# Kernel optimization log

Hardware: AMD Instinct MI355X
Metric: run time of the kernel (lower is better)

## Reference

```python
import jax, jax.numpy as jnp
import numpy as np
import math

IN_FEATURES = 512
RFF_FEATURES = 2048
OUT_FEATURES = 1000
N = 8192
RIDGE_PENALTY = 1.0
MEAN_FIELD_FACTOR = 25.0
RFF_SCALAR = math.sqrt(RFF_FEATURES / 2)  # 32.0


def _random_ortho(key, n, m):
    q, _ = jnp.linalg.qr(jax.random.normal(key, (n, m), dtype=jnp.float32))
    return q


def setup_inputs() -> dict:
    key = jax.random.key(0)
    k_d, k_w, k_norm, k_b, k_lw, k_lb, k_cov = jax.random.split(key, 7)
    D = jax.random.normal(k_d, (N, IN_FEATURES), dtype=jnp.float32)
    # RFF weight: concat of random orthonormal blocks (rff_features > in_features)
    ws = []
    dim_left = RFF_FEATURES
    kk = k_w
    while dim_left > IN_FEATURES:
        kk, sub = jax.random.split(kk)
        ws.append(_random_ortho(sub, IN_FEATURES, IN_FEATURES))
        dim_left -= IN_FEATURES
    kk, sub = jax.random.split(kk)
    ws.append(_random_ortho(sub, IN_FEATURES, dim_left))
    W = jnp.concatenate(ws, axis=1)  # [in, rff]
    feature_norm = jax.random.normal(k_norm, W.shape, dtype=jnp.float32) ** 2
    W = W * jnp.sqrt(feature_norm.sum(0))
    b = jax.random.uniform(k_b, (RFF_FEATURES,), dtype=jnp.float32) * (2.0 * math.pi)
    # logit head (nn.Linear): weight [out, rff], bias [out]
    bound = 1.0 / math.sqrt(RFF_FEATURES)
    logit_w = jax.random.uniform(k_lw, (OUT_FEATURES, RFF_FEATURES), dtype=jnp.float32,
                                 minval=-bound, maxval=bound)
    logit_b = jax.random.uniform(k_lb, (OUT_FEATURES,), dtype=jnp.float32,
                                 minval=-bound, maxval=bound)
    # positive-definite covariance buffer (stand-in for inverted precision)
    A = jax.random.normal(k_cov, (RFF_FEATURES, RFF_FEATURES), dtype=jnp.float32) * 0.01
    covariance = A @ A.T + jnp.eye(RFF_FEATURES, dtype=jnp.float32)
    return {"D": D, "W": W, "b": b, "logit_w": logit_w, "logit_b": logit_b,
            "covariance": covariance}


def reference(D, W, b, logit_w, logit_b, covariance):
    # RFF feature map: cos(D @ W + b) / rff_scalar  -> [N, rff]
    Phi = jnp.cos(D @ W + b) / RFF_SCALAR
    # linear head -> [N, out]
    pred = Phi @ logit_w.T + logit_b
    # diag(Phi @ cov @ Phi.T) * ridge computed row-wise in O(N*r^2)
    diag_cov = jnp.sum((Phi @ covariance) * Phi, axis=-1) * RIDGE_PENALTY  # [N]
    logits_scale = jnp.sqrt(1.0 + diag_cov * MEAN_FIELD_FACTOR)
    return pred / logits_scale[:, None]
```

## Files before the change

kernel.cpp:

```cpp
#include <hip/hip_runtime.h>
#include <hip/hip_fp8.h>
#include <math.h>

#define N_ROWS 8192
#define IN_F   512
#define RFF    2048
#define OUT_F  1000
#define OUT_PAD 1024
#define INV_RFF_SCALAR 0.03125f
#define MEAN_FIELD 25.0f
#define PHI_NT 24

typedef __attribute__((ext_vector_type(8))) short short8;
typedef __attribute__((ext_vector_type(4))) float f32x4;
typedef __attribute__((ext_vector_type(2))) long long2v;

__device__ __forceinline__ unsigned short f32_to_bf16(float f) {
    unsigned u = __float_as_uint(f);
    unsigned r = 0x7FFFu + ((u >> 16) & 1u);
    return (unsigned short)((u + r) >> 16);
}
__device__ __forceinline__ float bf16_to_f32(unsigned short h) {
    return __uint_as_float(((unsigned)h) << 16);
}
__device__ __forceinline__ unsigned char f32_to_fp8(float x) {
    __hip_fp8_e4m3 q(x);
    return (unsigned char)q.__x;
}

__device__ __forceinline__ int perm64(int k) {
    return (k & ~63) | (((k >> 3) & 3) << 4) | (((k >> 5) & 1) << 3) | (k & 7);
}

__device__ __forceinline__ void stage_tile8(const unsigned char* __restrict__ X,
                                            int r0, int k0b, unsigned char* lds,
                                            int w, int lane) {
    #pragma unroll
    for (int h = 0; h < 4; ++h) {
        int qb = h * 256 + w * 64;
        int q = qb + lane;
        int rt = q >> 7, c = (q >> 4) & 7, r = q & 15;
        const void* g = X + (size_t)(r0 + rt * 16 + r) * RFF + k0b + c * 16;
        __builtin_amdgcn_global_load_lds(
            (const __attribute__((address_space(1))) void*)g,
            (__attribute__((address_space(3))) void*)(lds + qb * 16),
            16, 0, 0);
    }
}

__device__ __forceinline__ void stage_tile64(const unsigned short* __restrict__ X,
                                             int r0, int k0, unsigned char* lds,
                                             int w, int lane) {
    #pragma unroll
    for (int h = 0; h < 4; ++h) {
        int qb = h * 256 + w * 64;
        int q = qb + lane;
        int rt = q >> 7, c = (q >> 4) & 7, r = q & 15;
        const void* g = X + (size_t)(r0 + rt * 16 + r) * RFF + k0 + c * 8;
        __builtin_amdgcn_global_load_lds(
            (const __attribute__((address_space(1))) void*)g,
            (__attribute__((address_space(3))) void*)(lds + qb * 16),
            16, 0, 0);
    }
}

__global__ __launch_bounds__(256) void mega_conv_kernel(
    const float* __restrict__ D, const float* __restrict__ W,
    const float* __restrict__ Lw, const float* __restrict__ cov,
    unsigned short* __restrict__ Dh, unsigned short* __restrict__ Dl,
    unsigned short* __restrict__ Wth, unsigned short* __restrict__ Wtl,
    unsigned short* __restrict__ Lw16, unsigned char* __restrict__ CovU8,
    float* __restrict__ Cd)
{
    __shared__ float tile[64][65];
    const int bid = blockIdx.x;
    const int tid = threadIdx.x;

    if (bid < 4096) {
        int i = bid * 256 + tid;
        float4 v = ((const float4*)D)[i];
        ushort4 h, l;
        h.x = f32_to_bf16(v.x); l.x = f32_to_bf16(v.x - bf16_to_f32(h.x));
        h.y = f32_to_bf16(v.y); l.y = f32_to_bf16(v.y - bf16_to_f32(h.y));
        h.z = f32_to_bf16(v.z); l.z = f32_to_bf16(v.z - bf16_to_f32(h.z));
        h.w = f32_to_bf16(v.w); l.w = f32_to_bf16(v.w - bf16_to_f32(h.w));
        ((ushort4*)Dh)[i] = h;
        ((ushort4*)Dl)[i] = l;
    } else if (bid < 4352) {
        int b = bid - 4096;
        const int n0 = (b & 31) * 64;
        const int k0 = (b >> 5) * 64;
        #pragma unroll
        for (int i = 0; i < 16; ++i) {
            int e = i * 256 + tid;
            int r = e >> 6, c = e & 63;
            tile[r][c] = W[(size_t)(k0 + r) * RFF + n0 + c];
        }
        __syncthreads();
        #pragma unroll
        for (int i = 0; i < 16; ++i) {
            int e = i * 256 + tid;
            int r = e >> 6, c = e & 63;
            float v = tile[c][r];
            unsigned short h = f32_to_bf16(v);
            unsigned short l = f32_to_bf16(v - bf16_to_f32(h));
            Wth[(size_t)(n0 + r) * IN_F + k0 + c] = h;
            Wtl[(size_t)(n0 + r) * IN_F + k0 + c] = l;
        }
    } else if (bid < 6400) {
        int i = (bid - 4352) * 256 + tid;
        int base = i * 4;
        int row = base >> 11;
        ushort4 o;
        if (row < OUT_F) {
            float4 v = ((const float4*)Lw)[i];
            o.x = f32_to_bf16(v.x); o.y = f32_to_bf16(v.y);
            o.z = f32_to_bf16(v.z); o.w = f32_to_bf16(v.w);
        } else {
            o.x = o.y = o.z = o.w = 0;
        }
        ((ushort4*)Lw16)[i] = o;
    } else {
        int i = (bid - 6400) * 256 + tid;
        int base = i * 4;
        int row = base >> 11;
        int col = base & 2047;
        int bn = row >> 7, bk = col >> 7;
        float w = (bk < bn) ? 16.0f : (bk == bn ? 8.0f : 0.0f);
        float4 v = ((const float4*)cov)[i];
        float vv[4] = {v.x, v.y, v.z, v.w};
        float wj[4];
        #pragma unroll
        for (int j = 0; j < 4; ++j) {
            if (col + j == row) { wj[j] = 0.0f; Cd[row] = vv[j]; }
            else wj[j] = w;
        }
        uchar4 o;
        o.x = f32_to_fp8(vv[0] * wj[0]); o.y = f32_to_fp8(vv[1] * wj[1]);
        o.z = f32_to_fp8(vv[2] * wj[2]); o.w = f32_to_fp8(vv[3] * wj[3]);
        *(uchar4*)(CovU8 + (size_t)row * RFF + perm64(col)) = o;
    }
}

__global__ __launch_bounds__(256) void conv_phi8_kernel(
    const unsigned short* __restrict__ Phi16, unsigned char* __restrict__ Phi8)
{
    int i = blockIdx.x * 256 + threadIdx.x;
    int base = i * 4;
    int row = base >> 11;
    int col = base & 2047;
    ushort4 v = ((const ushort4*)Phi16)[i];
    uchar4 o;
    o.x = f32_to_fp8(bf16_to_f32(v.x) * 32.0f);
    o.y = f32_to_fp8(bf16_to_f32(v.y) * 32.0f);
    o.z = f32_to_fp8(bf16_to_f32(v.z) * 32.0f);
    o.w = f32_to_fp8(bf16_to_f32(v.w) * 32.0f);
    *(uchar4*)(Phi8 + (size_t)row * RFF + perm64(col)) = o;
}


__device__ __forceinline__ void gload16u(const void* g, unsigned short* lds) {
    __builtin_amdgcn_global_load_lds(
        (const __attribute__((address_space(1))) void*)g,
        (__attribute__((address_space(3))) void*)lds, 16, 0, 0);
}

__device__ __forceinline__ void stage_ab(const unsigned short* __restrict__ src,
                                         int stride, int r0v, int kk,
                                         unsigned short* ldsbuf,
                                         int Qa, int h, int w, int lane) {
    int q   = w * 64 + lane;
    int RT  = h * 8 + Qa * 4 + (q >> 7);
    int c   = (q >> 4) & 7, r = q & 15;
    const void* g = src + (size_t)(r0v + RT * 16 + r) * stride + kk + c * 8;
    int RTu = h * 8 + Qa * 4 + (w >> 1);
    int cu  = (w & 1) * 4;
    gload16u(g, ldsbuf + RTu * 1024 + cu * 128);
}

__device__ __forceinline__ void stageB_g(const unsigned short* __restrict__ src,
                                         int cc0, int kk, unsigned short* ldsbuf,
                                         int nh, int h, int w, int lane) {
    int q    = w * 64 + lane;
    int i    = q >> 7;
    int RTp  = (i >> 1) * 4 + nh * 2 + (i & 1);
    int c    = (q >> 4) & 7, r = q & 15;
    const void* g = src + (size_t)(cc0 + h * 128 + RTp * 16 + r) * IN_F + kk + c * 8;
    int iu   = w >> 1;
    int RTpu = (iu >> 1) * 4 + nh * 2 + (iu & 1);
    int RTu  = h * 8 + RTpu;
    int cu   = (w & 1) * 4;
    gload16u(g, ldsbuf + RTu * 1024 + cu * 128);
}

#define SB0() __builtin_amdgcn_sched_barrier(0)
#define BARRIER() do { SB0(); __builtin_amdgcn_s_barrier(); SB0(); } while (0)
#define WAITVM(N) do { asm volatile("s_waitcnt vmcnt(" #N ")"); SB0(); } while (0)


#define READ_FA(FA, mh) do {                                                  \
    _Pragma("unroll")                                                         \
    for (int i_ = 0; i_ < 4; ++i_) {                                          \
        FA[i_][0] = *(const short8*)(A + (wm * 8 + (mh) * 4 + i_) * 1024      \
                                       + quad * 128 + ln * 8);                \
        FA[i_][1] = *(const short8*)(A + (wm * 8 + (mh) * 4 + i_) * 1024      \
                                       + 512 + quad * 128 + ln * 8);          \
    } } while (0)

#define READ_FB(FB, nh) do {                                                  \
    _Pragma("unroll")                                                         \
    for (int j_ = 0; j_ < 2; ++j_) {                                          \
        FB[j_][0] = *(const short8*)(B + (wn * 4 + (nh) * 2 + j_) * 1024      \
                                       + quad * 128 + ln * 8);                \
        FB[j_][1] = *(const short8*)(B + (wn * 4 + (nh) * 2 + j_) * 1024      \
                                       + 512 + quad * 128 + ln * 8);          \
    } } while (0)

#define MFMA16(MH, NH, FA, FB) do {                                           \
    __builtin_amdgcn_s_setprio(1);                                            \
    _Pragma("unroll")                                                         \
    for (int s_ = 0; s_ < 2; ++s_)                                            \
        _Pragma("unroll")                                                     \
        for (int i_ = 0; i_ < 4; ++i_)                                        \
            _Pragma("unroll")                                                 \
            for (int j_ = 0; j_ < 2; ++j_)                                    \
                acc[(MH) * 4 + i_][(NH) * 2 + j_] =                           \
                    __builtin_amdgcn_mfma_f32_16x16x32_bf16(                  \
                        FA[i_][s_], FB[j_][s_],                               \
                        acc[(MH) * 4 + i_][(NH) * 2 + j_], 0, 0, 0);          \
    __builtin_amdgcn_s_setprio(0);                                            \
} while (0)

__global__ __launch_bounds__(512, 2) void phi_mfma8p_kernel(
    const unsigned short* __restrict__ Dh, const unsigned short* __restrict__ Dl,
    const unsigned short* __restrict__ Wth, const unsigned short* __restrict__ Wtl,
    const float* __restrict__ bias, unsigned short* __restrict__ Phi)
{
    __shared__ unsigned short ldsA[2 * 16384];
    __shared__ unsigned short ldsB[2 * 16384];
    const int tid = threadIdx.x;
    const int w = tid >> 6, lane = tid & 63;
    const int wm = w >> 2, wn = w & 3;
    const int quad = lane >> 4, ln = lane & 15;

    const int bid = blockIdx.x;
    const int xcd = bid & 7, idx = bid >> 3;
    const int rb = (xcd >> 1) * 8 + (idx & 7);
    const int cb = (xcd & 1) * 4 + (idx >> 3);
    const int r0 = rb * 256;
    const int c0 = cb * 256;

    f32x4 acc[8][4];
    #pragma unroll
    for (int i = 0; i < 8; ++i)
        #pragma unroll
        for (int j = 0; j < 4; ++j)
            acc[i][j] = (f32x4)(0.0f);

    stage_ab(Dh, IN_F, r0, 0, ldsA, 0, 0, w, lane);
    stage_ab(Dh, IN_F, r0, 0, ldsA, 0, 1, w, lane);
    stage_ab(Dh, IN_F, r0, 0, ldsA, 1, 0, w, lane);
    stage_ab(Dh, IN_F, r0, 0, ldsA, 1, 1, w, lane);
    stageB_g(Wth, c0, 0, ldsB, 0, 0, w, lane);
    stageB_g(Wth, c0, 0, ldsB, 0, 1, w, lane);
    stageB_g(Wth, c0, 0, ldsB, 1, 0, w, lane);
    stageB_g(Wth, c0, 0, ldsB, 1, 1, w, lane);
    stage_ab(Dh, IN_F, r0, 64, ldsA + 16384, 0, 0, w, lane);
    stage_ab(Dh, IN_F, r0, 64, ldsA + 16384, 0, 1, w, lane);
    stageB_g(Wth, c0, 64, ldsB + 16384, 0, 0, w, lane);
    stageB_g(Wth, c0, 64, ldsB + 16384, 0, 1, w, lane);
    WAITVM(4);
    BARRIER();

    for (int t = 0; t < PHI_NT - 1; ++t) {
        const int buf = t & 1;
        const unsigned short* A = ldsA + buf * 16384;
        const unsigned short* B = ldsB + buf * 16384;
        unsigned short* curA = ldsA + buf * 16384;
        unsigned short* curB = ldsB + buf * 16384;
        unsigned short* othA = ldsA + (buf ^ 1) * 16384;
        unsigned short* othB = ldsB + (buf ^ 1) * 16384;
        const bool has2 = (t + 2) < PHI_NT;
        const int k1 = (t + 1) * 64, k2 = (t + 2) * 64;
        const int kk1 = k1 & 511, kk2 = k2 & 511;
        const unsigned short* A1 = (k1 >= 1024) ? Dl : Dh;
        const unsigned short* B1 = (k1 >= 1024) ? Wth : (k1 >= 512 ? Wtl : Wth);
        const unsigned short* A2 = (k2 >= 1024) ? Dl : Dh;
        const unsigned short* B2 = (k2 >= 1024) ? Wth : (k2 >= 512 ? Wtl : Wth);

        short8 fa[4][2], fb0[2][2], fb1[2][2];

        READ_FA(fa, 0);
        READ_FB(fb0, 0);
        stage_ab(A1, IN_F, r0, kk1, othA, 1, 0, w, lane);
        stage_ab(A1, IN_F, r0, kk1, othA, 1, 1, w, lane);
        BARRIER();
        MFMA16(0, 0, fa, fb0);
        BARRIER();

        READ_FB(fb1, 1);
        stageB_g(B1, c0, kk1, othB, 1, 0, w, lane);
        stageB_g(B1, c0, kk1, othB, 1, 1, w, lane);
        BARRIER();
        MFMA16(0, 1, fa, fb1);
        BARRIER();

        READ_FA(fa, 1);
        if (has2) { stage_ab(A2, IN_F, r0, kk2, curA, 0, 0, w, lane);
                    stage_ab(A2, IN_F, r0, kk2, curA, 0, 1, w, lane); }
        BARRIER();
        MFMA16(1, 0, fa, fb0);
        BARRIER();

        if (has2) { stageB_g(B2, c0, kk2, curB, 0, 0, w, lane);
                    stageB_g(B2, c0, kk2, curB, 0, 1, w, lane);
                    WAITVM(4); }
        else      { WAITVM(0); }
        BARRIER();
        MFMA16(1, 1, fa, fb1);
        BARRIER();
    }

    {
        asm volatile("" ::: "memory");
        const unsigned short* A = ldsA + ((PHI_NT - 1) & 1) * 16384;
        const unsigned short* B = ldsB + ((PHI_NT - 1) & 1) * 16384;
        short8 fa[4][2], fb0[2][2], fb1[2][2];
        READ_FA(fa, 0);
        READ_FB(fb0, 0);
        READ_FB(fb1, 1);
        MFMA16(0, 0, fa, fb0);
        MFMA16(0, 1, fa, fb1);
        READ_FA(fa, 1);
        MFMA16(1, 0, fa, fb0);
        MFMA16(1, 1, fa, fb1);
    }

    float bv[4];
    #pragma unroll
    for (int nt = 0; nt < 4; ++nt)
        bv[nt] = bias[c0 + wn * 64 + nt * 16 + ln];
    #pragma unroll
    for (int mt = 0; mt < 8; ++mt)
        #pragma unroll
        for (int nt = 0; nt < 4; ++nt) {
            int col = c0 + wn * 64 + nt * 16 + ln;
            #pragma unroll
            for (int reg = 0; reg < 4; ++reg) {
                int row = r0 + wm * 128 + mt * 16 + quad * 4 + reg;
                float z = acc[mt][nt][reg] + bv[nt];
                float p = __cosf(z) * INV_RFF_SCALAR;
                Phi[(size_t)row * RFF + col] = f32_to_bf16(p);
            }
        }
}

__global__ __launch_bounds__(256) void fused_dp_kernel(
    const unsigned char* __restrict__ Phi8, const unsigned char* __restrict__ CovU8,
    const unsigned short* __restrict__ Phi16, const float* __restrict__ Cd,
    float* __restrict__ diag, const unsigned short* __restrict__ Lw,
    float* __restrict__ out)
{
    __shared__ __align__(16) unsigned char ldsA[16384];
    __shared__ __align__(16) unsigned char ldsB[16384];
    const int bid = blockIdx.x;
    const int tid = threadIdx.x;
    const int w = tid >> 6, lane = tid & 63;
    const int wm = w >> 1, wn = w & 1;
    const int quad = lane >> 4, ln = lane & 15;
    const int m3 = bid % 3;

    if (m3 == 2) {
        const int pidx = bid / 3;
        const int r0 = (pidx >> 3) * 128;
        const int c0 = (pidx & 7) * 128;

        f32x4 acc[4][4];
        #pragma unroll
        for (int i = 0; i < 4; ++i)
            #pragma unroll
            for (int j = 0; j < 4; ++j)
                acc[i][j] = (f32x4)(0.0f);

        for (int k0 = 0; k0 < RFF; k0 += 64) {
            __syncthreads();
            stage_tile64(Phi16, r0, k0, ldsA, w, lane);
            stage_tile64(Lw,    c0, k0, ldsB, w, lane);
            __syncthreads();

            #pragma unroll
            for (int s = 0; s < 2; ++s) {
                short8 fa[4], fb[4];
                #pragma unroll
                for (int t = 0; t < 4; ++t) {
                    fa[t] = *(const short8*)(ldsA + (((wm * 4 + t) * 128 + (s * 4 + quad) * 16 + ln) << 4));
                    fb[t] = *(const short8*)(ldsB + (((wn * 4 + t) * 128 + (s * 4 + quad) * 16 + ln) << 4));
                }
                #pragma unroll
                for (int mt = 0; mt < 4; ++mt)
                    #pragma unroll
                    for (int nt = 0; nt < 4; ++nt)
                        acc[mt][nt] = __builtin_amdgcn_mfma_f32_16x16x32_bf16(
                            fa[mt], fb[nt], acc[mt][nt], 0, 0, 0);
            }
        }

        #pragma unroll
        for (int mt = 0; mt < 4; ++mt)
            #pragma unroll
            for (int nt = 0; nt < 4; ++nt) {
                int col = c0 + wn * 64 + nt * 16 + ln;
                if (col < OUT_F) {
                    #pragma unroll
                    for (int reg = 0; reg < 4; ++reg) {
                        int row = r0 + wm * 64 + mt * 16 + quad * 4 + reg;
                        out[(size_t)row * OUT_F + col] = acc[mt][nt][reg];
                    }
                }
            }
    } else {
        const int didx = (bid / 3) * 2 + m3;
        const int J = 15 - (didx & 15);
        const int r0 = (didx >> 4) * 128;
        const int c0 = J * 128;
        const int kmax = (J + 1) * 128;

        f32x4 acc[4][4];
        #pragma unroll
        for (int i = 0; i < 4; ++i)
            #pragma unroll
            for (int j = 0; j < 4; ++j)
                acc[i][j] = (f32x4)(0.0f);

        for (int k0 = 0; k0 < kmax; k0 += 128) {
            __syncthreads();
            stage_tile8(Phi8,  r0, k0, ldsA, w, lane);
            stage_tile8(CovU8, c0, k0, ldsB, w, lane);
            __syncthreads();

            #pragma unroll
            for (int kb = 0; kb < 2; ++kb) {
                long2v fa[4], fb[4];
                #pragma unroll
                for (int t = 0; t < 4; ++t) {
                    fa[t] = *(const long2v*)(ldsA + (((wm * 4 + t) * 128 + (kb * 4 + quad) * 16 + ln) << 4));
                    fb[t] = *(const long2v*)(ldsB + (((wn * 4 + t) * 128 + (kb * 4 + quad) * 16 + ln) << 4));
                }
                #pragma unroll
                for (int mt = 0; mt < 4; ++mt)
                    #pragma unroll
                    for (int nt = 0; nt < 4; ++nt)
                        acc[mt][nt] = __builtin_amdgcn_mfma_f32_16x16x32_fp8_fp8(
                            fa[mt].x, fb[nt].x, acc[mt][nt], 0, 0, 0);
                #pragma unroll
                for (int mt = 0; mt < 4; ++mt)
                    #pragma unroll
                    for (int nt = 0; nt < 4; ++nt)
                        acc[mt][nt] = __builtin_amdgcn_mfma_f32_16x16x32_fp8_fp8(
                            fa[mt].y, fb[nt].y, acc[mt][nt], 0, 0, 0);
            }
        }

        float cd[4];
        #pragma unroll
        for (int nt = 0; nt < 4; ++nt)
            cd[nt] = 256.0f * Cd[c0 + wn * 64 + nt * 16 + ln];
        #pragma unroll
        for (int mt = 0; mt < 4; ++mt) {
            float psum[4] = {0.f, 0.f, 0.f, 0.f};
            #pragma unroll
            for (int nt = 0; nt < 4; ++nt) {
                int col = c0 + wn * 64 + nt * 16 + ln;
                #pragma unroll
                for (int reg = 0; reg < 4; ++reg) {
                    int row = r0 + wm * 64 + mt * 16 + quad * 4 + reg;
                    float pv = bf16_to_f32(Phi16[(size_t)row * RFF + col]);
                    psum[reg] = fmaf(fmaf(cd[nt], pv, acc[mt][nt][reg]), pv, psum[reg]);
                }
            }
            #pragma unroll
            for (int off = 1; off < 16; off <<= 1)
                #pragma unroll
                for (int reg = 0; reg < 4; ++reg)
                    psum[reg] += __shfl_xor(psum[reg], off, 16);
            if (ln == 0) {
                #pragma unroll
                for (int reg = 0; reg < 4; ++reg) {
                    int row = r0 + wm * 64 + mt * 16 + quad * 4 + reg;
                    atomicAdd(&diag[row], psum[reg] * (1.0f / 256.0f));
                }
            }
        }
    }
}

__global__ __launch_bounds__(256) void pred_epilogue_kernel(
    float* __restrict__ out, const float* __restrict__ Lb,
    const float* __restrict__ diag)
{
    int i = blockIdx.x * 256 + threadIdx.x;
    int row = i / 250;
    int c = (i - row * 250) * 4;
    float s = 1.0f / sqrtf(1.0f + MEAN_FIELD * diag[row]);
    float4 v = *(float4*)(out + (size_t)row * OUT_F + c);
    float4 b = *(const float4*)(Lb + c);
    v.x = (v.x + b.x) * s;
    v.y = (v.y + b.y) * s;
    v.z = (v.z + b.z) * s;
    v.w = (v.w + b.w) * s;
    *(float4*)(out + (size_t)row * OUT_F + c) = v;
}

extern "C" void kernel_launch(void* const* d_in, const int* in_sizes, int n_in,
                              void* d_out, int out_size, void* d_ws, size_t ws_size,
                              hipStream_t stream) {
    const float* D    = (const float*)d_in[0];
    const float* W    = (const float*)d_in[1];
    const float* bias = (const float*)d_in[2];
    const float* Lw   = (const float*)d_in[3];
    const float* Lb   = (const float*)d_in[4];
    const float* cov  = (const float*)d_in[5];
    float* out = (float*)d_out;

    char* p = (char*)d_ws;
    unsigned short* Phi16 = (unsigned short*)p;  p += (size_t)N_ROWS * RFF * 2;
    unsigned char*  Phi8  = (unsigned char*)p;
    unsigned short* Dh    = (unsigned short*)p;  p += (size_t)N_ROWS * IN_F * 2;
    unsigned short* Dl    = (unsigned short*)p;  p += (size_t)N_ROWS * IN_F * 2;
    unsigned short* Wth   = (unsigned short*)p;  p += (size_t)RFF * IN_F * 2;
    unsigned short* Wtl   = (unsigned short*)p;  p += (size_t)RFF * IN_F * 2;
    unsigned short* Lw16  = (unsigned short*)p;  p += (size_t)OUT_PAD * RFF * 2;
    unsigned char*  CovU8 = (unsigned char*)p;
    float*          Cd    = (float*)(p + (size_t)RFF * RFF);
    p += (size_t)RFF * RFF * 2;
    float* diag           = (float*)p;

    hipMemsetAsync(diag, 0, N_ROWS * sizeof(float), stream);

    mega_conv_kernel<<<dim3(10496), dim3(256), 0, stream>>>(
        D, W, Lw, cov, Dh, Dl, Wth, Wtl, Lw16, CovU8, Cd);

    phi_mfma8p_kernel<<<dim3(256), dim3(512), 0, stream>>>(Dh, Dl, Wth, Wtl, bias, Phi16);
    conv_phi8_kernel<<<dim3(N_ROWS * RFF / 4 / 256), dim3(256), 0, stream>>>(Phi16, Phi8);

    fused_dp_kernel<<<dim3(1536), dim3(256), 0, stream>>>(
        Phi8, CovU8, Phi16, Cd, diag, Lw16, out);

    pred_epilogue_kernel<<<dim3(N_ROWS * 250 / 256), dim3(256), 0, stream>>>(out, Lb, diag);
}
```

Measured before the change: 327.1 us.

## Restructure pipeline: fuse Phi8 conversion with pred GEMM, fold epilogue into diag kernel

Removes the memset and standalone conv_phi8 and epilogue kernels. Diag zeroing and the counter reset move into the conversion megakernel. The pred GEMM becomes its own double-buffered 256x128-tile kernel whose extra blocks run the fp8 Phi conversion alongside it. The diag kernel ends with a per-row-block atomic counter so the last block applies bias and scaling, trading extra launches and a memory pass for a threadfence/counter protocol and different overlap between the pred and diag work.

New measurement: 505.8 us. 1.55x slower.

```diff
diff --git a/kernel.cpp b/kernel.cpp
--- a/kernel.cpp
+++ b/kernel.cpp
@@ -10,6 +10,7 @@
 #define INV_RFF_SCALAR 0.03125f
 #define MEAN_FIELD 25.0f
 #define PHI_NT 24
+#define PRED_NT 32
 
 typedef __attribute__((ext_vector_type(8))) short short8;
 typedef __attribute__((ext_vector_type(4))) float f32x4;
@@ -48,29 +49,13 @@
     }
 }
 
-__device__ __forceinline__ void stage_tile64(const unsigned short* __restrict__ X,
-                                             int r0, int k0, unsigned char* lds,
-                                             int w, int lane) {
-    #pragma unroll
-    for (int h = 0; h < 4; ++h) {
-        int qb = h * 256 + w * 64;
-        int q = qb + lane;
-        int rt = q >> 7, c = (q >> 4) & 7, r = q & 15;
-        const void* g = X + (size_t)(r0 + rt * 16 + r) * RFF + k0 + c * 8;
-        __builtin_amdgcn_global_load_lds(
-            (const __attribute__((address_space(1))) void*)g,
-            (__attribute__((address_space(3))) void*)(lds + qb * 16),
-            16, 0, 0);
-    }
-}
-
 __global__ __launch_bounds__(256) void mega_conv_kernel(
     const float* __restrict__ D, const float* __restrict__ W,
     const float* __restrict__ Lw, const float* __restrict__ cov,
     unsigned short* __restrict__ Dh, unsigned short* __restrict__ Dl,
     unsigned short* __restrict__ Wth, unsigned short* __restrict__ Wtl,
     unsigned short* __restrict__ Lw16, unsigned char* __restrict__ CovU8,
-    float* __restrict__ Cd)
+    float* __restrict__ Cd, float* __restrict__ diag, int* __restrict__ cnt)
 {
     __shared__ float tile[64][65];
     const int bid = blockIdx.x;
@@ -120,7 +105,7 @@
             o.x = o.y = o.z = o.w = 0;
         }
         ((ushort4*)Lw16)[i] = o;
-    } else {
+    } else if (bid < 10496) {
         int i = (bid - 6400) * 256 + tid;
         int base = i * 4;
         int row = base >> 11;
@@ -139,23 +124,12 @@
         o.x = f32_to_fp8(vv[0] * wj[0]); o.y = f32_to_fp8(vv[1] * wj[1]);
         o.z = f32_to_fp8(vv[2] * wj[2]); o.w = f32_to_fp8(vv[3] * wj[3]);
         *(uchar4*)(CovU8 + (size_t)row * RFF + perm64(col)) = o;
-    }
-}
-
-__global__ __launch_bounds__(256) void conv_phi8_kernel(
-    const unsigned short* __restrict__ Phi16, unsigned char* __restrict__ Phi8)
-{
-    int i = blockIdx.x * 256 + threadIdx.x;
-    int base = i * 4;
-    int row = base >> 11;
-    int col = base & 2047;
-    ushort4 v = ((const ushort4*)Phi16)[i];
-    uchar4 o;
-    o.x = f32_to_fp8(bf16_to_f32(v.x) * 32.0f);
-    o.y = f32_to_fp8(bf16_to_f32(v.y) * 32.0f);
-    o.z = f32_to_fp8(bf16_to_f32(v.z) * 32.0f);
-    o.w = f32_to_fp8(bf16_to_f32(v.w) * 32.0f);
-    *(uchar4*)(Phi8 + (size_t)row * RFF + perm64(col)) = o;
+    } else if (bid < 10504) {
+        int idx = (bid - 10496) * 256 + tid;
+        ((float4*)diag)[idx] = (float4){0.f, 0.f, 0.f, 0.f};
+    } else {
+        if (tid < 64) cnt[tid] = 0;
+    }
 }
 
 
@@ -355,160 +329,230 @@
         }
 }
 
-__global__ __launch_bounds__(256) void fused_dp_kernel(
+__global__ __launch_bounds__(512, 2) void pred_conv8_kernel(
+    const unsigned short* __restrict__ Phi, const unsigned short* __restrict__ Lw,
+    unsigned char* __restrict__ Phi8, float* __restrict__ out)
+{
+    __shared__ unsigned short ldsA[2 * 16384];
+    __shared__ unsigned short ldsB[2 * 8192];
+    const int tid = threadIdx.x;
+
+    if (blockIdx.x < 128) {
+        const int row0 = blockIdx.x * 64;
+        #pragma unroll 4
+        for (int e = tid; e < 64 * (RFF / 4); e += 512) {
+            int r = e >> 9;
+            int g = e & 511;
+            int row = row0 + r;
+            int col = g * 4;
+            ushort4 v = *(const ushort4*)(Phi + (size_t)row * RFF + col);
+            uchar4 o;
+            o.x = f32_to_fp8(bf16_to_f32(v.x) * 32.0f);
+            o.y = f32_to_fp8(bf16_to_f32(v.y) * 32.0f);
+            o.z = f32_to_fp8(bf16_to_f32(v.z) * 32.0f);
+            o.w = f32_to_fp8(bf16_to_f32(v.w) * 32.0f);
+            *(uchar4*)(Phi8 + (size_t)row * RFF + perm64(col)) = o;
+        }
+        return;
+    }
+
+    const int w = tid >> 6, lane = tid & 63;
+    const int wm = w >> 1, wn = w & 1;
+    const int quad = lane >> 4, ln = lane & 15;
+
+    const int pb = blockIdx.x - 128;
+    const int xcd = pb & 7, idx = pb >> 3;
+    const int rb = xcd * 4 + (idx >> 3);
+    const int cb = idx & 7;
+    const int r0 = rb * 256;
+    const int c0 = cb * 128;
+
+    f32x4 acc[4][4];
+    #pragma unroll
+    for (int i = 0; i < 4; ++i)
+        #pragma unroll
+        for (int j = 0; j < 4; ++j)
+            acc[i][j] = (f32x4)(0.0f);
+
+    stage_ab(Phi, RFF, r0, 0, ldsA, 0, 0, w, lane);
+    stage_ab(Phi, RFF, r0, 0, ldsA, 1, 0, w, lane);
+    stage_ab(Phi, RFF, r0, 0, ldsA, 0, 1, w, lane);
+    stage_ab(Phi, RFF, r0, 0, ldsA, 1, 1, w, lane);
+    stage_ab(Lw,  RFF, c0, 0, ldsB, 0, 0, w, lane);
+    stage_ab(Lw,  RFF, c0, 0, ldsB, 1, 0, w, lane);
+    WAITVM(0);
+    BARRIER();
+
+    for (int t = 0; t < PRED_NT; ++t) {
+        const int buf = t & 1;
+        const unsigned short* A = ldsA + buf * 16384;
+        const unsigned short* B = ldsB + buf * 8192;
+
+        if (t + 1 < PRED_NT) {
+            const int kk = (t + 1) * 64;
+            unsigned short* nA = ldsA + (buf ^ 1) * 16384;
+            unsigned short* nB = ldsB + (buf ^ 1) * 8192;
+            stage_ab(Phi, RFF, r0, kk, nA, 0, 0, w, lane);
+            stage_ab(Phi, RFF, r0, kk, nA, 1, 0, w, lane);
+            stage_ab(Phi, RFF, r0, kk, nA, 0, 1, w, lane);
+            stage_ab(Phi, RFF, r0, kk, nA, 1, 1, w, lane);
+            stage_ab(Lw,  RFF, c0, kk, nB, 0, 0, w, lane);
+            stage_ab(Lw,  RFF, c0, kk, nB, 1, 0, w, lane);
+        }
+
+        short8 fa[4][2], fb[4][2];
+        #pragma unroll
+        for (int i_ = 0; i_ < 4; ++i_) {
+            fa[i_][0] = *(const short8*)(A + (wm * 4 + i_) * 1024 + quad * 128 + ln * 8);
+            fa[i_][1] = *(const short8*)(A + (wm * 4 + i_) * 1024 + 512 + quad * 128 + ln * 8);
+        }
+        #pragma unroll
+        for (int j_ = 0; j_ < 4; ++j_) {
+            fb[j_][0] = *(const short8*)(B + (wn * 4 + j_) * 1024 + quad * 128 + ln * 8);
+            fb[j_][1] = *(const short8*)(B + (wn * 4 + j_) * 1024 + 512 + quad * 128 + ln * 8);
+        }
+        __builtin_amdgcn_s_setprio(1);
+        #pragma unroll
+        for (int s_ = 0; s_ < 2; ++s_)
+            #pragma unroll
+            for (int i_ = 0; i_ < 4; ++i_)
+                #pragma unroll
+                for (int j_ = 0; j_ < 4; ++j_)
+                    acc[i_][j_] = __builtin_amdgcn_mfma_f32_16x16x32_bf16(
+                        fa[i_][s_], fb[j_][s_], acc[i_][j_], 0, 0, 0);
+        __builtin_amdgcn_s_setprio(0);
+
+        WAITVM(0);
+        BARRIER();
+    }
+
+    #pragma unroll
+    for (int mt = 0; mt < 4; ++mt)
+        #pragma unroll
+        for (int nt = 0; nt < 4; ++nt) {
+            int col = c0 + wn * 64 + nt * 16 + ln;
+            if (col < OUT_F) {
+                #pragma unroll
+                for (int reg = 0; reg < 4; ++reg) {
+                    int row = r0 + wm * 64 + mt * 16 + quad * 4 + reg;
+                    out[(size_t)row * OUT_F + col] = acc[mt][nt][reg];
+                }
+            }
+        }
+}
+
+__global__ __launch_bounds__(256) void diag8_epi_kernel(
     const unsigned char* __restrict__ Phi8, const unsigned char* __restrict__ CovU8,
     const unsigned short* __restrict__ Phi16, const float* __restrict__ Cd,
-    float* __restrict__ diag, const unsigned short* __restrict__ Lw,
-    float* __restrict__ out)
+    float* __restrict__ diag, int* __restrict__ cnt,
+    float* __restrict__ out, const float* __restrict__ Lb)
 {
     __shared__ __align__(16) unsigned char ldsA[16384];
     __shared__ __align__(16) unsigned char ldsB[16384];
-    const int bid = blockIdx.x;
+    __shared__ float sS[128];
+    __shared__ int lastFlag;
     const int tid = threadIdx.x;
     const int w = tid >> 6, lane = tid & 63;
     const int wm = w >> 1, wn = w & 1;
     const int quad = lane >> 4, ln = lane & 15;
-    const int m3 = bid % 3;
-
-    if (m3 == 2) {
-        const int pidx = bid / 3;
-        const int r0 = (pidx >> 3) * 128;
-        const int c0 = (pidx & 7) * 128;
-
-        f32x4 acc[4][4];
-        #pragma unroll
-        for (int i = 0; i < 4; ++i)
-            #pragma unroll
-            for (int j = 0; j < 4; ++j)
-                acc[i][j] = (f32x4)(0.0f);
-
-        for (int k0 = 0; k0 < RFF; k0 += 64) {
-            __syncthreads();
-            stage_tile64(Phi16, r0, k0, ldsA, w, lane);
-            stage_tile64(Lw,    c0, k0, ldsB, w, lane);
-            __syncthreads();
-
-            #pragma unroll
-            for (int s = 0; s < 2; ++s) {
-                short8 fa[4], fb[4];
+    const int J = 15 - blockIdx.x;
+    const int r0 = blockIdx.y * 128;
+    const int c0 = J * 128;
+    const int kmax = (J + 1) * 128;
+
+    f32x4 acc[4][4];
+    #pragma unroll
+    for (int i = 0; i < 4; ++i)
+        #pragma unroll
+        for (int j = 0; j < 4; ++j)
+            acc[i][j] = (f32x4)(0.0f);
+
+    for (int k0 = 0; k0 < kmax; k0 += 128) {
+        __syncthreads();
+        stage_tile8(Phi8,  r0, k0, ldsA, w, lane);
+        stage_tile8(CovU8, c0, k0, ldsB, w, lane);
+        __syncthreads();
+
+        #pragma unroll
+        for (int kb = 0; kb < 2; ++kb) {
+            long2v fa[4], fb[4];
+            #pragma unroll
+            for (int t = 0; t < 4; ++t) {
+                fa[t] = *(const long2v*)(ldsA + (((wm * 4 + t) * 128 + (kb * 4 + quad) * 16 + ln) << 4));
+                fb[t] = *(const long2v*)(ldsB + (((wn * 4 + t) * 128 + (kb * 4 + quad) * 16 + ln) << 4));
+            }
+            #pragma unroll
+            for (int mt = 0; mt < 4; ++mt)
                 #pragma unroll
-                for (int t = 0; t < 4; ++t) {
-                    fa[t] = *(const short8*)(ldsA + (((wm * 4 + t) * 128 + (s * 4 + quad) * 16 + ln) << 4));
-                    fb[t] = *(const short8*)(ldsB + (((wn * 4 + t) * 128 + (s * 4 + quad) * 16 + ln) << 4));
-                }
+                for (int nt = 0; nt < 4; ++nt)
+                    acc[mt][nt] = __builtin_amdgcn_mfma_f32_16x16x32_fp8_fp8(
+                        fa[mt].x, fb[nt].x, acc[mt][nt], 0, 0, 0);
+            #pragma unroll
+            for (int mt = 0; mt < 4; ++mt)
                 #pragma unroll
-                for (int mt = 0; mt < 4; ++mt)
-                    #pragma unroll
-                    for (int nt = 0; nt < 4; ++nt)
-                        acc[mt][nt] = __builtin_amdgcn_mfma_f32_16x16x32_bf16(
-                            fa[mt], fb[nt], acc[mt][nt], 0, 0, 0);
+                for (int nt = 0; nt < 4; ++nt)
+                    acc[mt][nt] = __builtin_amdgcn_mfma_f32_16x16x32_fp8_fp8(
+                        fa[mt].y, fb[nt].y, acc[mt][nt], 0, 0, 0);
+        }
+    }
+
+    float cd[4];
+    #pragma unroll
+    for (int nt = 0; nt < 4; ++nt)
+        cd[nt] = 256.0f * Cd[c0 + wn * 64 + nt * 16 + ln];
+    #pragma unroll
+    for (int mt = 0; mt < 4; ++mt) {
+        float psum[4] = {0.f, 0.f, 0.f, 0.f};
+        #pragma unroll
+        for (int nt = 0; nt < 4; ++nt) {
+            int col = c0 + wn * 64 + nt * 16 + ln;
+            #pragma unroll
+            for (int reg = 0; reg < 4; ++reg) {
+                int row = r0 + wm * 64 + mt * 16 + quad * 4 + reg;
+                float pv = bf16_to_f32(Phi16[(size_t)row * RFF + col]);
+                psum[reg] = fmaf(fmaf(cd[nt], pv, acc[mt][nt][reg]), pv, psum[reg]);
             }
         }
-
-        #pragma unroll
-        for (int mt = 0; mt < 4; ++mt)
-            #pragma unroll
-            for (int nt = 0; nt < 4; ++nt) {
-                int col = c0 + wn * 64 + nt * 16 + ln;
-                if (col < OUT_F) {
-                    #pragma unroll
-                    for (int reg = 0; reg < 4; ++reg) {
-                        int row = r0 + wm * 64 + mt * 16 + quad * 4 + reg;
-                        out[(size_t)row * OUT_F + col] = acc[mt][nt][reg];
-                    }
-                }
+        #pragma unroll
+        for (int off = 1; off < 16; off <<= 1)
+            #pragma unroll
+            for (int reg = 0; reg < 4; ++reg)
+                psum[reg] += __shfl_xor(psum[reg], off, 16);
+        if (ln == 0) {
+            #pragma unroll
+            for (int reg = 0; reg < 4; ++reg) {
+                int row = r0 + wm * 64 + mt * 16 + quad * 4 + reg;
+                atomicAdd(&diag[row], psum[reg] * (1.0f / 256.0f));
             }
-    } else {
-        const int didx = (bid / 3) * 2 + m3;
-        const int J = 15 - (didx & 15);
-        const int r0 = (didx >> 4) * 128;
-        const int c0 = J * 128;
-        const int kmax = (J + 1) * 128;
-
-        f32x4 acc[4][4];
-        #pragma unroll
-        for (int i = 0; i < 4; ++i)
-            #pragma unroll
-            for (int j = 0; j < 4; ++j)
-                acc[i][j] = (f32x4)(0.0f);
-
-        for (int k0 = 0; k0 < kmax; k0 += 128) {
-            __syncthreads();
-            stage_tile8(Phi8,  r0, k0, ldsA, w, lane);
-            stage_tile8(CovU8, c0, k0, ldsB, w, lane);
-            __syncthreads();
-
-            #pragma unroll
-            for (int kb = 0; kb < 2; ++kb) {
-                long2v fa[4], fb[4];
-                #pragma unroll
-                for (int t = 0; t < 4; ++t) {
-                    fa[t] = *(const long2v*)(ldsA + (((wm * 4 + t) * 128 + (kb * 4 + quad) * 16 + ln) << 4));
-                    fb[t] = *(const long2v*)(ldsB + (((wn * 4 + t) * 128 + (kb * 4 + quad) * 16 + ln) << 4));
-                }
-                #pragma unroll
-                for (int mt = 0; mt < 4; ++mt)
-                    #pragma unroll
-                    for (int nt = 0; nt < 4; ++nt)
-                        acc[mt][nt] = __builtin_amdgcn_mfma_f32_16x16x32_fp8_fp8(
-                            fa[mt].x, fb[nt].x, acc[mt][nt], 0, 0, 0);
-                #pragma unroll
-                for (int mt = 0; mt < 4; ++mt)
-                    #pragma unroll
-                    for (int nt = 0; nt < 4; ++nt)
-                        acc[mt][nt] = __builtin_amdgcn_mfma_f32_16x16x32_fp8_fp8(
-                            fa[mt].y, fb[nt].y, acc[mt][nt], 0, 0, 0);
-            }
-        }
-
-        float cd[4];
-        #pragma unroll
-        for (int nt = 0; nt < 4; ++nt)
-            cd[nt] = 256.0f * Cd[c0 + wn * 64 + nt * 16 + ln];
-        #pragma unroll
-        for (int mt = 0; mt < 4; ++mt) {
-            float psum[4] = {0.f, 0.f, 0.f, 0.f};
-            #pragma unroll
-            for (int nt = 0; nt < 4; ++nt) {
-                int col = c0 + wn * 64 + nt * 16 + ln;
-                #pragma unroll
-                for (int reg = 0; reg < 4; ++reg) {
-                    int row = r0 + wm * 64 + mt * 16 + quad * 4 + reg;
-                    float pv = bf16_to_f32(Phi16[(size_t)row * RFF + col]);
-                    psum[reg] = fmaf(fmaf(cd[nt], pv, acc[mt][nt][reg]), pv, psum[reg]);
-                }
-            }
-            #pragma unroll
-            for (int off = 1; off < 16; off <<= 1)
-                #pragma unroll
-                for (int reg = 0; reg < 4; ++reg)
-                    psum[reg] += __shfl_xor(psum[reg], off, 16);
-            if (ln == 0) {
-                #pragma unroll
-                for (int reg = 0; reg < 4; ++reg) {
-                    int row = r0 + wm * 64 + mt * 16 + quad * 4 + reg;
-                    atomicAdd(&diag[row], psum[reg] * (1.0f / 256.0f));
-                }
-            }
-        }
-    }
-}
-
-__global__ __launch_bounds__(256) void pred_epilogue_kernel(
-    float* __restrict__ out, const float* __restrict__ Lb,
-    const float* __restrict__ diag)
-{
-    int i = blockIdx.x * 256 + threadIdx.x;
-    int row = i / 250;
-    int c = (i - row * 250) * 4;
-    float s = 1.0f / sqrtf(1.0f + MEAN_FIELD * diag[row]);
-    float4 v = *(float4*)(out + (size_t)row * OUT_F + c);
-    float4 b = *(const float4*)(Lb + c);
-    v.x = (v.x + b.x) * s;
-    v.y = (v.y + b.y) * s;
-    v.z = (v.z + b.z) * s;
-    v.w = (v.w + b.w) * s;
-    *(float4*)(out + (size_t)row * OUT_F + c) = v;
+        }
+    }
+
+    __syncthreads();
+    __threadfence();
+    if (tid == 0)
+        lastFlag = (atomicAdd(&cnt[blockIdx.y], 1) == 15) ? 1 : 0;
+    __syncthreads();
+    if (lastFlag) {
+        if (tid < 128) {
+            float dv = atomicAdd(&diag[r0 + tid], 0.0f);
+            sS[tid] = 1.0f / sqrtf(1.0f + MEAN_FIELD * dv);
+        }
+        __syncthreads();
+        for (int e = tid; e < 128 * 250; e += 256) {
+            int rr = e / 250;
+            int ccg = e - rr * 250;
+            int cc = ccg * 4;
+            int row = r0 + rr;
+            float s = sS[rr];
+            float4 v = *(float4*)(out + (size_t)row * OUT_F + cc);
+            float4 b = *(const float4*)(Lb + cc);
+            v.x = (v.x + b.x) * s;
+            v.y = (v.y + b.y) * s;
+            v.z = (v.z + b.z) * s;
+            v.w = (v.w + b.w) * s;
+            *(float4*)(out + (size_t)row * OUT_F + cc) = v;
+        }
+    }
 }
 
 extern "C" void kernel_launch(void* const* d_in, const int* in_sizes, int n_in,
@@ -532,19 +576,17 @@
     unsigned short* Lw16  = (unsigned short*)p;  p += (size_t)OUT_PAD * RFF * 2;
     unsigned char*  CovU8 = (unsigned char*)p;
     float*          Cd    = (float*)(p + (size_t)RFF * RFF);
+    int*            cnt   = (int*)(p + (size_t)RFF * RFF + 8192);
     p += (size_t)RFF * RFF * 2;
     float* diag           = (float*)p;
 
-    hipMemsetAsync(diag, 0, N_ROWS * sizeof(float), stream);
-
-    mega_conv_kernel<<<dim3(10496), dim3(256), 0, stream>>>(
-        D, W, Lw, cov, Dh, Dl, Wth, Wtl, Lw16, CovU8, Cd);
+    mega_conv_kernel<<<dim3(10505), dim3(256), 0, stream>>>(
+        D, W, Lw, cov, Dh, Dl, Wth, Wtl, Lw16, CovU8, Cd, diag, cnt);
 
     phi_mfma8p_kernel<<<dim3(256), dim3(512), 0, stream>>>(Dh, Dl, Wth, Wtl, bias, Phi16);
-    conv_phi8_kernel<<<dim3(N_ROWS * RFF / 4 / 256), dim3(256), 0, stream>>>(Phi16, Phi8);
-
-    fused_dp_kernel<<<dim3(1536), dim3(256), 0, stream>>>(
-        Phi8, CovU8, Phi16, Cd, diag, Lw16, out);
-
-    pred_epilogue_kernel<<<dim3(N_ROWS * 250 / 256), dim3(256), 0, stream>>>(out, Lb, diag);
-}
+
+    pred_conv8_kernel<<<dim3(384), dim3(512), 0, stream>>>(Phi16, Lw16, Phi8, out);
+
+    diag8_epi_kernel<<<dim3(16, 64), dim3(256), 0, stream>>>(
+        Phi8, CovU8, Phi16, Cd, diag, cnt, out, Lb);
+}
```
